# Optimization experiments

Measured on AMD Instinct MI355X. Metric: run time of the kernel, lower is better.

Reference implementation:

```python
import jax, jax.numpy as jnp
import numpy as np

IN_DIM = 1024
HEAD_DIM = 64
NUM_HEADS = 16
SEQ = 4096


def setup_inputs() -> dict:
    key = jax.random.key(0)
    ks = jax.random.split(key, 7)
    s = 1.0 / np.sqrt(IN_DIM)
    return {
        "h": jax.random.normal(ks[0], (SEQ, IN_DIM), dtype=jnp.float32),
        "Wq": jax.random.uniform(ks[1], (IN_DIM, NUM_HEADS * HEAD_DIM), jnp.float32, -s, s),
        "Wk": jax.random.uniform(ks[2], (IN_DIM, NUM_HEADS * HEAD_DIM), jnp.float32, -s, s),
        "Wv": jax.random.uniform(ks[3], (IN_DIM, NUM_HEADS * HEAD_DIM), jnp.float32, -s, s),
        "bq": jax.random.uniform(ks[4], (NUM_HEADS * HEAD_DIM,), jnp.float32, -s, s),
        "bk": jax.random.uniform(ks[5], (NUM_HEADS * HEAD_DIM,), jnp.float32, -s, s),
        "bv": jax.random.uniform(ks[6], (NUM_HEADS * HEAD_DIM,), jnp.float32, -s, s),
    }


def reference(h, Wq, Wk, Wv, bq, bk, bv):
    n = h.shape[0]
    # QKV projections -> [H, S, D]
    q = (h @ Wq + bq).reshape(n, NUM_HEADS, HEAD_DIM).transpose(1, 0, 2)
    k = (h @ Wk + bk).reshape(n, NUM_HEADS, HEAD_DIM).transpose(1, 0, 2)
    v = (h @ Wv + bv).reshape(n, NUM_HEADS, HEAD_DIM).transpose(1, 0, 2)
    scale = 1.0 / np.sqrt(HEAD_DIM).astype(np.float32)
    scores = jnp.einsum('hsd,htd->hst', q, k) * scale  # [H, S, S]
    probs = jax.nn.softmax(scores, axis=-1)
    out = jnp.einsum('hst,htd->hsd', probs, v)  # [H, S, D]
    return out.transpose(1, 0, 2).reshape(n, NUM_HEADS * HEAD_DIM)
```

## Files before the change

### kernel.cpp

```cpp
#include <hip/hip_runtime.h>
#include <hip/hip_bf16.h>

#define IN_DIM    1024
#define HEAD_DIM  64
#define NUM_HEADS 16
#define SEQ       4096

#define QSCALE 0.18033688011112042f

typedef __bf16 bf16;
typedef __attribute__((ext_vector_type(4))) __bf16 bf16x4;
typedef __attribute__((ext_vector_type(8))) __bf16 bf16x8;
typedef __attribute__((ext_vector_type(4))) float floatx4;

__device__ __forceinline__ void async16(bf16* lds, const bf16* g) {
    __builtin_amdgcn_global_load_lds(
        (const __attribute__((address_space(1))) unsigned int*)g,
        (__attribute__((address_space(3))) unsigned int*)lds, 16, 0, 0);
}


__global__ void mha_conv_h(const float* __restrict__ h, bf16* __restrict__ hb) {
    int i = blockIdx.x * blockDim.x + threadIdx.x;
    float4 v = ((const float4*)h)[i];
    bf16x4 r;
    r[0] = (bf16)v.x; r[1] = (bf16)v.y; r[2] = (bf16)v.z; r[3] = (bf16)v.w;
    ((bf16x4*)hb)[i] = r;
}

__global__ void mha_conv_wt(const float* __restrict__ Wq, const float* __restrict__ Wk,
                            const float* __restrict__ Wv, bf16* __restrict__ Wt) {
    __shared__ bf16 tile[64][65];
    const int mat = blockIdx.z;
    const float* W = (mat == 0) ? Wq : (mat == 1) ? Wk : Wv;
    const int k0 = blockIdx.y * 64, n0 = blockIdx.x * 64;
    const int tn = threadIdx.x & 63, tq = threadIdx.x >> 6;
#pragma unroll
    for (int i = 0; i < 16; ++i) {
        int kk = tq + i * 4;
        tile[kk][tn] = (bf16)W[(size_t)(k0 + kk) * 1024 + n0 + tn];
    }
    __syncthreads();
#pragma unroll
    for (int i = 0; i < 16; ++i) {
        int nn = tq + i * 4;
        Wt[((size_t)mat << 20) + (size_t)(n0 + nn) * 1024 + k0 + tn] = tile[tn][nn];
    }
}

__launch_bounds__(256)
__global__ void mha_qkv_gemm(const bf16* __restrict__ hb, const bf16* __restrict__ Wt,
                             const float* __restrict__ bq, const float* __restrict__ bk,
                             const float* __restrict__ bv,
                             bf16* __restrict__ Qb, bf16* __restrict__ Kb,
                             bf16* __restrict__ Vt) {
    __shared__ __align__(16) bf16 As[128 * 32];
    __shared__ __align__(16) bf16 Bs[128 * 32];

    const int lane = threadIdx.x & 63;
    const int wave = threadIdx.x >> 6;
    const int l16  = lane & 15;
    const int quad = lane >> 4;
    const int wm   = wave & 1;
    const int wn   = wave >> 1;

    const int m0  = blockIdx.x * 128;
    const int n0  = blockIdx.y * 128;
    const int mat = n0 >> 10;
    const int nc0 = n0 & 1023;

    const bf16* Wp = Wt + ((size_t)mat << 20);

    floatx4 acc[4][4] = {};
    const int swz = (l16 >> 1) & 3;

    int g0 = wave * 128 + lane, g1 = g0 + 64;
    int row0 = g0 >> 2, gc0 = (g0 & 3) ^ ((row0 >> 1) & 3);
    int row1 = g1 >> 2, gc1 = (g1 & 3) ^ ((row1 >> 1) & 3);
    bf16* la0 = As + (size_t)(wave * 128) * 8;
    bf16* la1 = As + (size_t)(wave * 128 + 64) * 8;
    bf16* lb0 = Bs + (size_t)(wave * 128) * 8;
    bf16* lb1 = Bs + (size_t)(wave * 128 + 64) * 8;

    if (mat != 2) {
        for (int k0 = 0; k0 < IN_DIM; k0 += 32) {
            async16(la0, hb + (size_t)(m0 + row0) * IN_DIM + k0 + gc0 * 8);
            async16(la1, hb + (size_t)(m0 + row1) * IN_DIM + k0 + gc1 * 8);
            async16(lb0, Wp + (size_t)(nc0 + row0) * IN_DIM + k0 + gc0 * 8);
            async16(lb1, Wp + (size_t)(nc0 + row1) * IN_DIM + k0 + gc1 * 8);
            __syncthreads();
            bf16x8 af[4], bf[4];
#pragma unroll
            for (int mt = 0; mt < 4; ++mt)
                af[mt] = *(const bf16x8*)(As + (size_t)(wm * 64 + mt * 16 + l16) * 32
                                          + ((quad ^ swz) * 8));
#pragma unroll
            for (int nt = 0; nt < 4; ++nt)
                bf[nt] = *(const bf16x8*)(Bs + (size_t)(wn * 64 + nt * 16 + l16) * 32
                                          + ((quad ^ swz) * 8));
#pragma unroll
            for (int mt = 0; mt < 4; ++mt)
#pragma unroll
                for (int nt = 0; nt < 4; ++nt)
                    acc[mt][nt] = __builtin_amdgcn_mfma_f32_16x16x32_bf16(af[mt], bf[nt],
                                                                          acc[mt][nt], 0, 0, 0);
            __syncthreads();
        }
        const float* bias = (mat == 0) ? bq : bk;
#pragma unroll
        for (int nt = 0; nt < 4; ++nt) {
            int nc = nc0 + wn * 64 + nt * 16 + l16;
            float bb = bias[nc];
            int head = nc >> 6, d = nc & 63;
#pragma unroll
            for (int mt = 0; mt < 4; ++mt)
#pragma unroll
                for (int r = 0; r < 4; ++r) {
                    int srow = m0 + wm * 64 + mt * 16 + quad * 4 + r;
                    float v = acc[mt][nt][r] + bb;
                    if (mat == 0)
                        Qb[((size_t)head * SEQ + srow) * HEAD_DIM + d] = (bf16)(v * QSCALE);
                    else
                        Kb[((size_t)head * SEQ + srow) * HEAD_DIM + d] = (bf16)v;
                }
        }
    } else {
        for (int k0 = 0; k0 < IN_DIM; k0 += 32) {
            async16(la0, hb + (size_t)(m0 + row0) * IN_DIM + k0 + gc0 * 8);
            async16(la1, hb + (size_t)(m0 + row1) * IN_DIM + k0 + gc1 * 8);
            async16(lb0, Wp + (size_t)(nc0 + row0) * IN_DIM + k0 + gc0 * 8);
            async16(lb1, Wp + (size_t)(nc0 + row1) * IN_DIM + k0 + gc1 * 8);
            __syncthreads();
            bf16x8 af[4], bf[4];
#pragma unroll
            for (int mt = 0; mt < 4; ++mt)
                af[mt] = *(const bf16x8*)(As + (size_t)(wm * 64 + mt * 16 + l16) * 32
                                          + ((quad ^ swz) * 8));
#pragma unroll
            for (int nt = 0; nt < 4; ++nt)
                bf[nt] = *(const bf16x8*)(Bs + (size_t)(wn * 64 + nt * 16 + l16) * 32
                                          + ((quad ^ swz) * 8));
#pragma unroll
            for (int mt = 0; mt < 4; ++mt)
#pragma unroll
                for (int nt = 0; nt < 4; ++nt)
                    acc[mt][nt] = __builtin_amdgcn_mfma_f32_16x16x32_bf16(bf[nt], af[mt],
                                                                          acc[mt][nt], 0, 0, 0);
            __syncthreads();
        }
#pragma unroll
        for (int nt = 0; nt < 4; ++nt)
#pragma unroll
            for (int r = 0; r < 4; ++r) {
                int n = nc0 + wn * 64 + nt * 16 + quad * 4 + r;
                float bb = bv[n];
                int head = n >> 6, d = n & 63;
#pragma unroll
                for (int mt = 0; mt < 4; ++mt) {
                    int s = m0 + wm * 64 + mt * 16 + l16;
                    Vt[((size_t)head * 64 + d) * SEQ + s] = (bf16)(acc[mt][nt][r] + bb);
                }
            }
    }
}

__launch_bounds__(256, 2)
__global__ void mha_attn(const bf16* __restrict__ Qb, const bf16* __restrict__ Kb,
                         const bf16* __restrict__ Vt, float* __restrict__ out) {
    __shared__ __align__(16) bf16 Ks[2][64 * 64];
    __shared__ __align__(16) bf16 Vs[2][64 * 64];
    __shared__ __align__(16) bf16 Ps[16][16 * 72];

    const int lane = threadIdx.x & 63;
    const int wave = threadIdx.x >> 6;
    const int l16  = lane & 15;
    const int quad = lane >> 4;

    const int hh    = blockIdx.y;
    const int qbase = blockIdx.x * 256 + wave * 64;

    const bf16* Qh = Qb + (size_t)hh * SEQ * HEAD_DIM;
    const bf16* Kh = Kb + (size_t)hh * SEQ * HEAD_DIM;
    const bf16* Vh = Vt + (size_t)hh * HEAD_DIM * SEQ;

    const int g0 = wave * 128 + lane, g1 = g0 + 64;
    const int sr0 = g0 >> 3, sc0 = (g0 & 7) ^ (sr0 & 7);
    const int sr1 = g1 >> 3, sc1 = (g1 & 7) ^ (sr1 & 7);

    bf16x8 qf[4][2];
#pragma unroll
    for (int m = 0; m < 4; ++m)
#pragma unroll
        for (int ks = 0; ks < 2; ++ks)
            qf[m][ks] = *(const bf16x8*)(Qh + (size_t)(qbase + m * 16 + l16) * HEAD_DIM
                                         + ks * 32 + quad * 8);

    bf16x8 vone;
#pragma unroll
    for (int i = 0; i < 8; ++i) vone[i] = (bf16)1.0f;

    floatx4 o[4][4] = {};
    floatx4 ol[4]   = {};

    const int swk = l16 & 7;

    auto stage = [&](int slot, int t) {
        async16(&Ks[slot][(wave * 128) * 8],      Kh + (size_t)(t * 64 + sr0) * HEAD_DIM + sc0 * 8);
        async16(&Ks[slot][(wave * 128 + 64) * 8], Kh + (size_t)(t * 64 + sr1) * HEAD_DIM + sc1 * 8);
        async16(&Vs[slot][(wave * 128) * 8],      Vh + (size_t)sr0 * SEQ + t * 64 + sc0 * 8);
        async16(&Vs[slot][(wave * 128 + 64) * 8], Vh + (size_t)sr1 * SEQ + t * 64 + sc1 * 8);
    };

    stage(0, 0);
    __syncthreads();

    for (int t = 0; t < 64; ++t) {
        const int cur = t & 1;
        if (t < 63) stage(cur ^ 1, t + 1);

        bf16x8 kf[4][2];
#pragma unroll
        for (int tt = 0; tt < 4; ++tt)
#pragma unroll
            for (int ks = 0; ks < 2; ++ks)
                kf[tt][ks] = *(const bf16x8*)(&Ks[cur][(size_t)(tt * 16 + l16) * 64
                                              + (((ks * 4 + quad) ^ swk) * 8)]);
#pragma unroll
        for (int m = 0; m < 4; ++m) {
            bf16* lp = &Ps[wave * 4 + m][0];
#pragma unroll
            for (int tt = 0; tt < 4; ++tt) {
                floatx4 s = {};
                s = __builtin_amdgcn_mfma_f32_16x16x32_bf16(kf[tt][0], qf[m][0], s, 0, 0, 0);
                s = __builtin_amdgcn_mfma_f32_16x16x32_bf16(kf[tt][1], qf[m][1], s, 0, 0, 0);
                bf16x4 pk;
#pragma unroll
                for (int r = 0; r < 4; ++r) pk[r] = (bf16)__builtin_amdgcn_exp2f(s[r]);
                *(bf16x4*)(lp + l16 * 72 + tt * 16 + quad * 4) = pk;
            }
        }

        bf16x8 vf[4][2];
#pragma unroll
        for (int dt = 0; dt < 4; ++dt)
#pragma unroll
            for (int ks = 0; ks < 2; ++ks)
                vf[dt][ks] = *(const bf16x8*)(&Vs[cur][(size_t)(dt * 16 + l16) * 64
                                              + (((ks * 4 + quad) ^ swk) * 8)]);
#pragma unroll
        for (int m = 0; m < 4; ++m) {
            bf16* lp = &Ps[wave * 4 + m][0];
#pragma unroll
            for (int ks = 0; ks < 2; ++ks) {
                bf16x8 pf = *(const bf16x8*)(lp + l16 * 72 + ks * 32 + quad * 8);
#pragma unroll
                for (int dt = 0; dt < 4; ++dt)
                    o[m][dt] = __builtin_amdgcn_mfma_f32_16x16x32_bf16(pf, vf[dt][ks],
                                                                       o[m][dt], 0, 0, 0);
                ol[m] = __builtin_amdgcn_mfma_f32_16x16x32_bf16(pf, vone, ol[m], 0, 0, 0);
            }
        }
        __syncthreads();
    }

#pragma unroll
    for (int m = 0; m < 4; ++m)
#pragma unroll
        for (int r = 0; r < 4; ++r) {
            float inv = 1.0f / ol[m][r];
            int srow_o = qbase + m * 16 + quad * 4 + r;
#pragma unroll
            for (int dt = 0; dt < 4; ++dt)
                out[(size_t)srow_o * (NUM_HEADS * HEAD_DIM) + hh * 64 + dt * 16 + l16]
                    = o[m][dt][r] * inv;
        }
}

extern "C" void kernel_launch(void* const* d_in, const int* in_sizes, int n_in,
                              void* d_out, int out_size, void* d_ws, size_t ws_size,
                              hipStream_t stream) {
    const float* h  = (const float*)d_in[0];
    const float* Wq = (const float*)d_in[1];
    const float* Wk = (const float*)d_in[2];
    const float* Wv = (const float*)d_in[3];
    const float* bq = (const float*)d_in[4];
    const float* bk = (const float*)d_in[5];
    const float* bv = (const float*)d_in[6];
    float* out = (float*)d_out;

    char* ws = (char*)d_ws;
    const size_t MB = 1024 * 1024;
    bf16* hb = (bf16*)(ws);
    bf16* Wt = (bf16*)(ws + 8 * MB);
    bf16* Qb = (bf16*)(ws + 14 * MB);
    bf16* Kb = (bf16*)(ws + 22 * MB);
    bf16* Vt = (bf16*)(ws + 30 * MB);

    mha_conv_h<<<(SEQ * IN_DIM / 4) / 256, 256, 0, stream>>>(h, hb);
    mha_conv_wt<<<dim3(16, 16, 3), 256, 0, stream>>>(Wq, Wk, Wv, Wt);
    mha_qkv_gemm<<<dim3(SEQ / 128, (3 * IN_DIM) / 128), 256, 0, stream>>>(
        hb, Wt, bq, bk, bv, Qb, Kb, Vt);
    mha_attn<<<dim3(SEQ / 256, NUM_HEADS), 256, 0, stream>>>(Qb, Kb, Vt, out);
}
```

Baseline: 233.1 us.

## Split attention over the key dimension into two partitions and add a combine kernel

```diff
diff --git a/kernel.cpp b/kernel.cpp
--- a/kernel.cpp
+++ b/kernel.cpp
@@ -164,9 +164,11 @@
     }
 }
 
+template<int TS>
 __launch_bounds__(256, 2)
 __global__ void mha_attn(const bf16* __restrict__ Qb, const bf16* __restrict__ Kb,
-                         const bf16* __restrict__ Vt, float* __restrict__ out) {
+                         const bf16* __restrict__ Vt, float* __restrict__ Op,
+                         float* __restrict__ Lp, float* __restrict__ out) {
     __shared__ __align__(16) bf16 Ks[2][64 * 64];
     __shared__ __align__(16) bf16 Vs[2][64 * 64];
     __shared__ __align__(16) bf16 Ps[16][16 * 72];
@@ -177,7 +179,10 @@
     const int quad = lane >> 4;
 
     const int hh    = blockIdx.y;
+    const int zz    = blockIdx.z;
     const int qbase = blockIdx.x * 256 + wave * 64;
+    const int tbase = zz * (64 / TS);
+    const int niter = 64 / TS;
 
     const bf16* Qh = Qb + (size_t)hh * SEQ * HEAD_DIM;
     const bf16* Kh = Kb + (size_t)hh * SEQ * HEAD_DIM;
@@ -211,12 +216,12 @@
         async16(&Vs[slot][(wave * 128 + 64) * 8], Vh + (size_t)sr1 * SEQ + t * 64 + sc1 * 8);
     };
 
-    stage(0, 0);
+    stage(0, tbase);
     __syncthreads();
 
-    for (int t = 0; t < 64; ++t) {
+    for (int t = 0; t < niter; ++t) {
         const int cur = t & 1;
-        if (t < 63) stage(cur ^ 1, t + 1);
+        if (t < niter - 1) stage(cur ^ 1, tbase + t + 1);
 
         bf16x8 kf[4][2];
 #pragma unroll
@@ -263,17 +268,49 @@
         __syncthreads();
     }
 
-#pragma unroll
-    for (int m = 0; m < 4; ++m)
-#pragma unroll
-        for (int r = 0; r < 4; ++r) {
-            float inv = 1.0f / ol[m][r];
-            int srow_o = qbase + m * 16 + quad * 4 + r;
-#pragma unroll
-            for (int dt = 0; dt < 4; ++dt)
-                out[(size_t)srow_o * (NUM_HEADS * HEAD_DIM) + hh * 64 + dt * 16 + l16]
-                    = o[m][dt][r] * inv;
-        }
+    if (TS == 1) {
+#pragma unroll
+        for (int m = 0; m < 4; ++m)
+#pragma unroll
+            for (int r = 0; r < 4; ++r) {
+                float inv = 1.0f / ol[m][r];
+                int srow = qbase + m * 16 + quad * 4 + r;
+#pragma unroll
+                for (int dt = 0; dt < 4; ++dt)
+                    out[(size_t)srow * (NUM_HEADS * HEAD_DIM) + hh * 64 + dt * 16 + l16]
+                        = o[m][dt][r] * inv;
+            }
+    } else {
+        float* Oz = Op + ((size_t)(zz * NUM_HEADS + hh) * SEQ) * HEAD_DIM;
+        float* Lz = Lp + (size_t)(zz * NUM_HEADS + hh) * SEQ;
+#pragma unroll
+        for (int m = 0; m < 4; ++m)
+#pragma unroll
+            for (int r = 0; r < 4; ++r) {
+                int srow = qbase + m * 16 + quad * 4 + r;
+#pragma unroll
+                for (int dt = 0; dt < 4; ++dt)
+                    Oz[(size_t)srow * HEAD_DIM + dt * 16 + l16] = o[m][dt][r];
+                if (l16 == 0) Lz[srow] = ol[m][r];
+            }
+    }
+}
+
+__global__ void mha_combine(const float* __restrict__ Op, const float* __restrict__ Lp,
+                            float* __restrict__ out) {
+    int i = blockIdx.x * blockDim.x + threadIdx.x;
+    int j = i * 4;
+    int s = j >> 10, rem = j & 1023, hh = rem >> 6, d = rem & 63;
+    size_t i0 = ((size_t)hh * SEQ + s) * HEAD_DIM + d;
+    size_t i1 = ((size_t)(NUM_HEADS + hh) * SEQ + s) * HEAD_DIM + d;
+    float4 a = *(const float4*)(Op + i0);
+    float4 b = *(const float4*)(Op + i1);
+    float l = Lp[(size_t)hh * SEQ + s] + Lp[(size_t)(NUM_HEADS + hh) * SEQ + s];
+    float inv = 1.0f / l;
+    float4 r;
+    r.x = (a.x + b.x) * inv; r.y = (a.y + b.y) * inv;
+    r.z = (a.z + b.z) * inv; r.w = (a.w + b.w) * inv;
+    *(float4*)(out + j) = r;
 }
 
 extern "C" void kernel_launch(void* const* d_in, const int* in_sizes, int n_in,
@@ -290,15 +327,28 @@
 
     char* ws = (char*)d_ws;
     const size_t MB = 1024 * 1024;
-    bf16* hb = (bf16*)(ws);
-    bf16* Wt = (bf16*)(ws + 8 * MB);
-    bf16* Qb = (bf16*)(ws + 14 * MB);
-    bf16* Kb = (bf16*)(ws + 22 * MB);
-    bf16* Vt = (bf16*)(ws + 30 * MB);
+    bf16* Qb = (bf16*)(ws);
+    bf16* Kb = (bf16*)(ws + 8 * MB);
+    bf16* Vt = (bf16*)(ws + 16 * MB);
+    bf16* hb = (bf16*)(ws + 24 * MB);
+    bf16* Wt = (bf16*)(ws + 32 * MB);
+    float* Op = (float*)(ws + 24 * MB);
+    float* Lp = (float*)(ws + 24 * MB + (size_t)2 * NUM_HEADS * SEQ * HEAD_DIM * 4);
+
+    const size_t NEED = 24 * MB + (size_t)2 * NUM_HEADS * SEQ * HEAD_DIM * 4
+                      + (size_t)2 * NUM_HEADS * SEQ * 4;
+    const bool split = (ws_size >= NEED);
 
     mha_conv_h<<<(SEQ * IN_DIM / 4) / 256, 256, 0, stream>>>(h, hb);
     mha_conv_wt<<<dim3(16, 16, 3), 256, 0, stream>>>(Wq, Wk, Wv, Wt);
     mha_qkv_gemm<<<dim3(SEQ / 128, (3 * IN_DIM) / 128), 256, 0, stream>>>(
         hb, Wt, bq, bk, bv, Qb, Kb, Vt);
-    mha_attn<<<dim3(SEQ / 256, NUM_HEADS), 256, 0, stream>>>(Qb, Kb, Vt, out);
-}
+    if (split) {
+        mha_attn<2><<<dim3(SEQ / 256, NUM_HEADS, 2), 256, 0, stream>>>(
+            Qb, Kb, Vt, Op, Lp, out);
+        mha_combine<<<(SEQ * IN_DIM / 4) / 256, 256, 0, stream>>>(Op, Lp, out);
+    } else {
+        mha_attn<1><<<dim3(SEQ / 256, NUM_HEADS, 1), 256, 0, stream>>>(
+            Qb, Kb, Vt, Op, Lp, out);
+    }
+}
```

New measurement: 212.5 us. 1.1x faster.
